# Optimization experiments

Hardware: AMD Instinct MI355X
Metric: run time of the kernel (lower is better)

The kernel has to match this reference:

```python
import jax, jax.numpy as jnp
import numpy as np

B, W, F = 64, 128, 64          # batch, window (node feat dim), n_features (nodes)
H, OUTW = 4, 128               # num_heads, out window size
NEG_SLOPE = 0.2                # LeakyReLU negative slope (alpha)


def setup_inputs() -> dict:
    key = jax.random.key(0)
    ks = jax.random.split(key, 6)
    scale_in = 1.0 / np.sqrt(W)
    scale_a = 1.0 / np.sqrt(OUTW)
    return {
        "x": jax.random.normal(ks[0], (B, W, F), dtype=jnp.float32),
        "W_src": jax.random.normal(ks[1], (H * OUTW, W), dtype=jnp.float32) * scale_in,
        "b_src": jnp.zeros((H * OUTW,), dtype=jnp.float32),
        "W_dst": jax.random.normal(ks[2], (H * OUTW, W), dtype=jnp.float32) * scale_in,
        "b_dst": jnp.zeros((H * OUTW,), dtype=jnp.float32),
        "attn": jax.random.normal(ks[3], (H, OUTW), dtype=jnp.float32) * scale_a,
    }


def reference(x, W_src, b_src, W_dst, b_dst, attn):
    # x: [B, W, F] -> node features nf: [B, F, W] (F nodes, W-dim features)
    nf = jnp.transpose(x, (0, 2, 1))
    b, f, w = nf.shape
    h, outw = attn.shape
    # GATv2 separate source/destination projections (share_weights=False)
    fs = (nf @ W_src.T + b_src).reshape(b, f, h, outw)  # [B, F, H, outW]
    fd = (nf @ W_dst.T + b_dst).reshape(b, f, h, outw)
    # additive score over complete graph with self-loops: e[b,i,j,h,d]
    s = fs[:, :, None, :, :] + fd[:, None, :, :, :]      # [B, src, dst, H, outW]
    e = jnp.where(s >= 0, s, NEG_SLOPE * s)              # LeakyReLU
    scores = jnp.einsum('bijhd,hd->bhij', e, attn)       # [B, H, src, dst]
    # edge softmax: normalize over incoming edges (sources) per destination
    a = jax.nn.softmax(scores, axis=2)
    # weighted scatter-sum aggregation at destinations
    out = jnp.einsum('bhij,bihd->bjhd', a, fs)           # [B, F, H, outW]
    out = out.mean(axis=2)                               # mean over heads -> [B, F, outW]
    return jnp.transpose(out, (0, 2, 1))                 # [B, outW, F]
```

## Files before the change

### kernel.cpp

```cpp
#include <hip/hip_runtime.h>
#include <math.h>

#define BB 64
#define WW 128
#define FF 64
#define HH 4
#define OW 128

__global__ __launch_bounds__(256) void gat_proj(
    const float* __restrict__ x,
    const float* __restrict__ Wsrc,
    const float* __restrict__ bsrc,
    const float* __restrict__ Wdst,
    const float* __restrict__ bdst,
    float* __restrict__ fs,
    float* __restrict__ fd)
{
    __shared__ float xl[64 * FF];
    __shared__ float wl[64 * 68];
    __shared__ float bl[64];

    const int b  = blockIdx.x >> 4;
    const int rt = blockIdx.x & 15;
    const bool is_src = rt < 8;
    const int rm0 = (rt & 7) * 64;

    const float* Wm = is_src ? Wsrc : Wdst;
    const float* bm = is_src ? bsrc : bdst;

    const int t  = threadIdx.x;
    const int f0 = (t & 15) * 4;
    const int r0 = (t >> 4) * 4;

    float acc[4][4] = {};

    for (int kp = 0; kp < 2; ++kp) {
        {
            const float4* xs = (const float4*)(x + (size_t)b * (WW * FF) + kp * 64 * FF);
            float4* xd = (float4*)xl;
            #pragma unroll
            for (int p = 0; p < 4; ++p)
                xd[p * 256 + t] = xs[p * 256 + t];
            float4* wd = (float4*)wl;
            #pragma unroll
            for (int p = 0; p < 4; ++p) {
                int idx = p * 256 + t;
                int r = idx >> 4, kq = idx & 15;
                wd[r * 17 + kq] =
                    *(const float4*)(Wm + (size_t)(rm0 + r) * WW + kp * 64 + kq * 4);
            }
            if (kp == 0 && t < 64) bl[t] = bm[rm0 + t];
        }
        __syncthreads();

        #pragma unroll
        for (int k0 = 0; k0 < 64; k0 += 4) {
            float4 xv[4], wv[4];
            #pragma unroll
            for (int kk = 0; kk < 4; ++kk)
                xv[kk] = *(const float4*)&xl[(k0 + kk) * FF + f0];
            #pragma unroll
            for (int rr = 0; rr < 4; ++rr)
                wv[rr] = *(const float4*)&wl[(r0 + rr) * 68 + k0];
            #pragma unroll
            for (int kk = 0; kk < 4; ++kk) {
                #pragma unroll
                for (int rr = 0; rr < 4; ++rr) {
                    const float wf = ((const float*)&wv[rr])[kk];
                    const float* xf = (const float*)&xv[kk];
                    acc[rr][0] = fmaf(xf[0], wf, acc[rr][0]);
                    acc[rr][1] = fmaf(xf[1], wf, acc[rr][1]);
                    acc[rr][2] = fmaf(xf[2], wf, acc[rr][2]);
                    acc[rr][3] = fmaf(xf[3], wf, acc[rr][3]);
                }
            }
        }
        __syncthreads();
    }

    const int h  = (rt & 7) >> 1;
    const int d0 = ((rt & 1) * 64) + r0;
    float* dst = (is_src ? fs : fd) + (((size_t)b * HH + h) * FF) * OW;
    float b0 = bl[r0 + 0], b1 = bl[r0 + 1], b2 = bl[r0 + 2], b3 = bl[r0 + 3];
    #pragma unroll
    for (int ff = 0; ff < 4; ++ff) {
        float4 o;
        o.x = acc[0][ff] + b0;
        o.y = acc[1][ff] + b1;
        o.z = acc[2][ff] + b2;
        o.w = acc[3][ff] + b3;
        *(float4*)&dst[(size_t)(f0 + ff) * OW + d0] = o;
    }
}

__global__ __launch_bounds__(256) void gat_attn(
    const float* __restrict__ fs,
    const float* __restrict__ fd,
    const float* __restrict__ attn,
    float* __restrict__ ws2)
{
    __shared__ float fsl[FF * 132];
    __shared__ float fdl[32 * 132];
    __shared__ float St[FF * 36];
    __shared__ float A6[OW], B4[OW];
    __shared__ float cs[FF], cd[32];
    __shared__ float redm[8][32];
    __shared__ float reds[8][32];
    __shared__ float invl[32];

    const int bx = blockIdx.x;
    const int jh = bx & 1;
    const int h  = (bx >> 1) & 3;
    const int b  = bx >> 3;
    const size_t bh = (size_t)b * HH + h;
    const int jbase = jh * 32;

    const int t    = threadIdx.x;
    const int wv   = t >> 6;
    const int lane = t & 63;

    {
        const float4* s = (const float4*)(fs + bh * (FF * OW));
        float4* d4 = (float4*)fsl;
        #pragma unroll
        for (int p = 0; p < 8; ++p) {
            int idx = p * 256 + t;
            int i = idx >> 5, kq = idx & 31;
            d4[i * 33 + kq] = s[idx];
        }
        const float4* fsrc = (const float4*)(fd + (bh * FF + jbase) * OW);
        float4* fdst = (float4*)fdl;
        #pragma unroll
        for (int p = 0; p < 4; ++p) {
            int idx = p * 256 + t;
            int j = idx >> 5, kq = idx & 31;
            fdst[j * 33 + kq] = fsrc[idx];
        }
        if (t < 128) {
            float a = attn[h * OW + t];
            A6[t] = 0.6f * a;
            B4[t] = 0.4f * a;
        }
    }
    __syncthreads();

    if (t < 64) {
        float s = 0.0f;
        #pragma unroll 8
        for (int c = 0; c < 32; ++c) {
            float4 fv = *(const float4*)&fsl[t * 132 + c * 4];
            float4 av = *(const float4*)&A6[c * 4];
            s = fmaf(fv.x, av.x, fmaf(fv.y, av.y, fmaf(fv.z, av.z, fmaf(fv.w, av.w, s))));
        }
        cs[t] = s;
    } else if (t < 96) {
        const int j = t - 64;
        float s = 0.0f;
        #pragma unroll 8
        for (int c = 0; c < 32; ++c) {
            float4 fv = *(const float4*)&fdl[j * 132 + c * 4];
            float4 av = *(const float4*)&A6[c * 4];
            s = fmaf(fv.x, av.x, fmaf(fv.y, av.y, fmaf(fv.z, av.z, fmaf(fv.w, av.w, s))));
        }
        cd[j] = s;
    }
    __syncthreads();

    const int jl0 = wv * 8;
    {
        float sc[8] = {};
        #pragma unroll 4
        for (int c = 0; c < 32; ++c) {
            const int d0 = c * 4;
            float4 fsv = *(const float4*)&fsl[lane * 132 + d0];
            float4 b4  = *(const float4*)&B4[d0];
            #pragma unroll
            for (int jj = 0; jj < 8; ++jj) {
                float4 fdv = *(const float4*)&fdl[(jl0 + jj) * 132 + d0];
                float r = sc[jj];
                r = fmaf(b4.x, fabsf(fsv.x + fdv.x), r);
                r = fmaf(b4.y, fabsf(fsv.y + fdv.y), r);
                r = fmaf(b4.z, fabsf(fsv.z + fdv.z), r);
                r = fmaf(b4.w, fabsf(fsv.w + fdv.w), r);
                sc[jj] = r;
            }
        }
        const float csl = cs[lane];
        float4 o0, o1;
        o0.x = sc[0] + csl + cd[jl0 + 0];
        o0.y = sc[1] + csl + cd[jl0 + 1];
        o0.z = sc[2] + csl + cd[jl0 + 2];
        o0.w = sc[3] + csl + cd[jl0 + 3];
        o1.x = sc[4] + csl + cd[jl0 + 4];
        o1.y = sc[5] + csl + cd[jl0 + 5];
        o1.z = sc[6] + csl + cd[jl0 + 6];
        o1.w = sc[7] + csl + cd[jl0 + 7];
        *(float4*)&St[lane * 36 + jl0]     = o0;
        *(float4*)&St[lane * 36 + jl0 + 4] = o1;
    }
    __syncthreads();

    {
        const int j = t & 31, st = t >> 5;
        const int i0 = st * 8;
        float m = St[i0 * 36 + j];
        #pragma unroll
        for (int k = 1; k < 8; ++k) m = fmaxf(m, St[(i0 + k) * 36 + j]);
        redm[st][j] = m;
    }
    __syncthreads();
    {
        const int j = t & 31, st = t >> 5;
        const int i0 = st * 8;
        float mj = redm[0][j];
        #pragma unroll
        for (int s2 = 1; s2 < 8; ++s2) mj = fmaxf(mj, redm[s2][j]);
        float ps = 0.0f;
        #pragma unroll
        for (int k = 0; k < 8; ++k) {
            float e = __expf(St[(i0 + k) * 36 + j] - mj);
            St[(i0 + k) * 36 + j] = e;
            ps += e;
        }
        reds[st][j] = ps;
    }
    __syncthreads();
    if (t < 32) {
        float l = 0.0f;
        #pragma unroll
        for (int s2 = 0; s2 < 8; ++s2) l += reds[s2][t];
        invl[t] = 0.25f / l;
    }
    __syncthreads();

    {
        const int dg = t & 7;
        const int jr = t >> 3;
        float ag[16] = {};
        for (int i = 0; i < FF; ++i) {
            const float p = St[i * 36 + jr];
            const float* fr = &fsl[i * 132 + dg * 4];
            float4 f0 = *(const float4*)(fr);
            float4 f1 = *(const float4*)(fr + 32);
            float4 f2 = *(const float4*)(fr + 64);
            float4 f3 = *(const float4*)(fr + 96);
            ag[0]  = fmaf(p, f0.x, ag[0]);  ag[1]  = fmaf(p, f0.y, ag[1]);
            ag[2]  = fmaf(p, f0.z, ag[2]);  ag[3]  = fmaf(p, f0.w, ag[3]);
            ag[4]  = fmaf(p, f1.x, ag[4]);  ag[5]  = fmaf(p, f1.y, ag[5]);
            ag[6]  = fmaf(p, f1.z, ag[6]);  ag[7]  = fmaf(p, f1.w, ag[7]);
            ag[8]  = fmaf(p, f2.x, ag[8]);  ag[9]  = fmaf(p, f2.y, ag[9]);
            ag[10] = fmaf(p, f2.z, ag[10]); ag[11] = fmaf(p, f2.w, ag[11]);
            ag[12] = fmaf(p, f3.x, ag[12]); ag[13] = fmaf(p, f3.y, ag[13]);
            ag[14] = fmaf(p, f3.z, ag[14]); ag[15] = fmaf(p, f3.w, ag[15]);
        }
        const float iv = invl[jr];
        float* wout = ws2 + (bh * FF + jbase + jr) * OW + dg * 4;
        #pragma unroll
        for (int q = 0; q < 4; ++q) {
            float4 o;
            o.x = ag[q * 4 + 0] * iv;
            o.y = ag[q * 4 + 1] * iv;
            o.z = ag[q * 4 + 2] * iv;
            o.w = ag[q * 4 + 3] * iv;
            *(float4*)&wout[q * 32] = o;
        }
    }
}

__global__ __launch_bounds__(256) void gat_reduce(
    const float* __restrict__ ws2,
    float* __restrict__ out)
{
    __shared__ float tl[16][132];
    const int b  = blockIdx.x >> 2;
    const int jg = blockIdx.x & 3;
    const int t  = threadIdx.x;

    const float* base = ws2 + ((size_t)b * HH * FF + jg * 16) * OW;
    #pragma unroll
    for (int p = 0; p < 2; ++p) {
        int idx = p * 256 + t;
        int j = idx >> 5, q = idx & 31;
        const float* src = base + (size_t)j * OW + q * 4;
        float4 s0 = *(const float4*)(src);
        float4 s1 = *(const float4*)(src + (size_t)FF * OW);
        float4 s2 = *(const float4*)(src + (size_t)2 * FF * OW);
        float4 s3 = *(const float4*)(src + (size_t)3 * FF * OW);
        float4 o;
        o.x = s0.x + s1.x + s2.x + s3.x;
        o.y = s0.y + s1.y + s2.y + s3.y;
        o.z = s0.z + s1.z + s2.z + s3.z;
        o.w = s0.w + s1.w + s2.w + s3.w;
        *(float4*)&tl[j][q * 4] = o;
    }
    __syncthreads();
    #pragma unroll
    for (int it = 0; it < 8; ++it) {
        int idx = it * 256 + t;
        int j = idx & 15, d = idx >> 4;
        out[((size_t)b * OW + d) * FF + jg * 16 + j] = tl[j][d];
    }
}

extern "C" void kernel_launch(void* const* d_in, const int* in_sizes, int n_in,
                              void* d_out, int out_size, void* d_ws, size_t ws_size,
                              hipStream_t stream) {
    const float* x    = (const float*)d_in[0];
    const float* Wsrc = (const float*)d_in[1];
    const float* bsrc = (const float*)d_in[2];
    const float* Wdst = (const float*)d_in[3];
    const float* bdst = (const float*)d_in[4];
    const float* attn = (const float*)d_in[5];
    float* out = (float*)d_out;

    const size_t SL = (size_t)BB * HH * FF * OW;
    float* fs  = (float*)d_ws;
    float* fd  = fs + SL;
    float* ws2 = fd + SL;

    gat_proj  <<<BB * 16,     256, 0, stream>>>(x, Wsrc, bsrc, Wdst, bdst, fs, fd);
    gat_attn  <<<BB * HH * 2, 256, 0, stream>>>(fs, fd, attn, ws2);
    gat_reduce<<<BB * 4,      256, 0, stream>>>(ws2, out);
}
```

Before: 114.9 us.

## Fuse projection, attention and head-reduction into one kernel with atomic output

Merges the three kernels into one kernel per (batch, head) block. Each block computes the src/dst projections straight into shared memory, which a union reuses for the attention stage, then handles all 64 destinations in a single 512-thread block. Head averaging becomes atomicAdd into a zeroed output. This drops the global round trips for fs/fd/ws2 and two kernel launches. In exchange it adds a memset, contention on the atomics, the output reduction order varies across heads, and there are fewer, larger blocks (256).

```diff
diff --git a/kernel.cpp b/kernel.cpp
--- a/kernel.cpp
+++ b/kernel.cpp
@@ -7,139 +7,108 @@
 #define HH 4
 #define OW 128
 
-__global__ __launch_bounds__(256) void gat_proj(
+
+struct GemmRegion {
+    float xq[32 * 64];
+    float wq[2 * 128 * 36];
+};
+struct AttnRegion {
+    float fsl[64 * 132];
+    float fdl[64 * 132];
+    float st[64 * 68];
+    float A6[OW], B4[OW];
+    float cs[FF], cd[FF];
+    float redm[8 * 64];
+    float reds[8 * 64];
+    float invl[64];
+};
+union SMem { GemmRegion g; AttnRegion a; };
+
+__global__ __launch_bounds__(512) void gat_fused(
     const float* __restrict__ x,
     const float* __restrict__ Wsrc,
     const float* __restrict__ bsrc,
     const float* __restrict__ Wdst,
     const float* __restrict__ bdst,
-    float* __restrict__ fs,
-    float* __restrict__ fd)
+    const float* __restrict__ attn,
+    float* __restrict__ out)
 {
-    __shared__ float xl[64 * FF];
-    __shared__ float wl[64 * 68];
-    __shared__ float bl[64];
-
-    const int b  = blockIdx.x >> 4;
-    const int rt = blockIdx.x & 15;
-    const bool is_src = rt < 8;
-    const int rm0 = (rt & 7) * 64;
-
-    const float* Wm = is_src ? Wsrc : Wdst;
-    const float* bm = is_src ? bsrc : bdst;
-
+    __shared__ __align__(16) SMem sm;
+    __shared__ float bl[2 * 128];
+
+    const int bx = blockIdx.x;
+    const int h  = bx & 3;
+    const int b  = bx >> 2;
     const int t  = threadIdx.x;
-    const int f0 = (t & 15) * 4;
-    const int r0 = (t >> 4) * 4;
-
-    float acc[4][4] = {};
-
-    for (int kp = 0; kp < 2; ++kp) {
+
+    const int m  = t >> 8;
+    const int i0 = (t & 15) * 4;
+    const int d0 = ((t >> 4) & 15) * 8;
+
+    if (t < 256) bl[t] = (t & 128 ? bdst : bsrc)[h * 128 + (t & 127)];
+
+    float acc[8][4] = {};
+
+    for (int kq = 0; kq < 4; ++kq) {
+        if (kq) __syncthreads();
         {
-            const float4* xs = (const float4*)(x + (size_t)b * (WW * FF) + kp * 64 * FF);
-            float4* xd = (float4*)xl;
-            #pragma unroll
-            for (int p = 0; p < 4; ++p)
-                xd[p * 256 + t] = xs[p * 256 + t];
-            float4* wd = (float4*)wl;
-            #pragma unroll
-            for (int p = 0; p < 4; ++p) {
-                int idx = p * 256 + t;
-                int r = idx >> 4, kq = idx & 15;
-                wd[r * 17 + kq] =
-                    *(const float4*)(Wm + (size_t)(rm0 + r) * WW + kp * 64 + kq * 4);
-            }
-            if (kp == 0 && t < 64) bl[t] = bm[rm0 + t];
+            const float4* xs = (const float4*)(x + ((size_t)b * WW + kq * 32) * FF);
+            ((float4*)sm.g.xq)[t] = xs[t];
+        }
+        #pragma unroll
+        for (int p = 0; p < 4; ++p) {
+            int idx = p * 512 + t;
+            int mm = idx >> 10, d = (idx >> 3) & 127, q = idx & 7;
+            const float* src = (mm ? Wdst : Wsrc)
+                             + (size_t)(h * 128 + d) * WW + kq * 32 + q * 4;
+            *(float4*)&sm.g.wq[(mm * 128 + d) * 36 + q * 4] = *(const float4*)src;
         }
         __syncthreads();
 
         #pragma unroll
-        for (int k0 = 0; k0 < 64; k0 += 4) {
-            float4 xv[4], wv[4];
+        for (int k0 = 0; k0 < 32; k0 += 4) {
+            float4 xv[4];
             #pragma unroll
             for (int kk = 0; kk < 4; ++kk)
-                xv[kk] = *(const float4*)&xl[(k0 + kk) * FF + f0];
-            #pragma unroll
-            for (int rr = 0; rr < 4; ++rr)
-                wv[rr] = *(const float4*)&wl[(r0 + rr) * 68 + k0];
+                xv[kk] = *(const float4*)&sm.g.xq[(k0 + kk) * 64 + i0];
+            float4 wv[8];
+            #pragma unroll
+            for (int dd = 0; dd < 8; ++dd)
+                wv[dd] = *(const float4*)&sm.g.wq[(m * 128 + d0 + dd) * 36 + k0];
             #pragma unroll
             for (int kk = 0; kk < 4; ++kk) {
+                const float* xf = (const float*)&xv[kk];
                 #pragma unroll
-                for (int rr = 0; rr < 4; ++rr) {
-                    const float wf = ((const float*)&wv[rr])[kk];
-                    const float* xf = (const float*)&xv[kk];
-                    acc[rr][0] = fmaf(xf[0], wf, acc[rr][0]);
-                    acc[rr][1] = fmaf(xf[1], wf, acc[rr][1]);
-                    acc[rr][2] = fmaf(xf[2], wf, acc[rr][2]);
-                    acc[rr][3] = fmaf(xf[3], wf, acc[rr][3]);
+                for (int dd = 0; dd < 8; ++dd) {
+                    const float wf = ((const float*)&wv[dd])[kk];
+                    acc[dd][0] = fmaf(xf[0], wf, acc[dd][0]);
+                    acc[dd][1] = fmaf(xf[1], wf, acc[dd][1]);
+                    acc[dd][2] = fmaf(xf[2], wf, acc[dd][2]);
+                    acc[dd][3] = fmaf(xf[3], wf, acc[dd][3]);
                 }
             }
         }
-        __syncthreads();
-    }
-
-    const int h  = (rt & 7) >> 1;
-    const int d0 = ((rt & 1) * 64) + r0;
-    float* dst = (is_src ? fs : fd) + (((size_t)b * HH + h) * FF) * OW;
-    float b0 = bl[r0 + 0], b1 = bl[r0 + 1], b2 = bl[r0 + 2], b3 = bl[r0 + 3];
-    #pragma unroll
-    for (int ff = 0; ff < 4; ++ff) {
-        float4 o;
-        o.x = acc[0][ff] + b0;
-        o.y = acc[1][ff] + b1;
-        o.z = acc[2][ff] + b2;
-        o.w = acc[3][ff] + b3;
-        *(float4*)&dst[(size_t)(f0 + ff) * OW + d0] = o;
-    }
-}
-
-__global__ __launch_bounds__(256) void gat_attn(
-    const float* __restrict__ fs,
-    const float* __restrict__ fd,
-    const float* __restrict__ attn,
-    float* __restrict__ ws2)
-{
-    __shared__ float fsl[FF * 132];
-    __shared__ float fdl[32 * 132];
-    __shared__ float St[FF * 36];
-    __shared__ float A6[OW], B4[OW];
-    __shared__ float cs[FF], cd[32];
-    __shared__ float redm[8][32];
-    __shared__ float reds[8][32];
-    __shared__ float invl[32];
-
-    const int bx = blockIdx.x;
-    const int jh = bx & 1;
-    const int h  = (bx >> 1) & 3;
-    const int b  = bx >> 3;
-    const size_t bh = (size_t)b * HH + h;
-    const int jbase = jh * 32;
-
-    const int t    = threadIdx.x;
-    const int wv   = t >> 6;
-    const int lane = t & 63;
-
-    {
-        const float4* s = (const float4*)(fs + bh * (FF * OW));
-        float4* d4 = (float4*)fsl;
-        #pragma unroll
-        for (int p = 0; p < 8; ++p) {
-            int idx = p * 256 + t;
-            int i = idx >> 5, kq = idx & 31;
-            d4[i * 33 + kq] = s[idx];
-        }
-        const float4* fsrc = (const float4*)(fd + (bh * FF + jbase) * OW);
-        float4* fdst = (float4*)fdl;
-        #pragma unroll
-        for (int p = 0; p < 4; ++p) {
-            int idx = p * 256 + t;
-            int j = idx >> 5, kq = idx & 31;
-            fdst[j * 33 + kq] = fsrc[idx];
+    }
+    __syncthreads();
+
+    {
+        float* dst = m ? sm.a.fdl : sm.a.fsl;
+        #pragma unroll
+        for (int ii = 0; ii < 4; ++ii) {
+            #pragma unroll
+            for (int dq = 0; dq < 2; ++dq) {
+                float4 o;
+                o.x = acc[dq * 4 + 0][ii] + bl[m * 128 + d0 + dq * 4 + 0];
+                o.y = acc[dq * 4 + 1][ii] + bl[m * 128 + d0 + dq * 4 + 1];
+                o.z = acc[dq * 4 + 2][ii] + bl[m * 128 + d0 + dq * 4 + 2];
+                o.w = acc[dq * 4 + 3][ii] + bl[m * 128 + d0 + dq * 4 + 3];
+                *(float4*)&dst[(i0 + ii) * 132 + d0 + dq * 4] = o;
+            }
         }
         if (t < 128) {
-            float a = attn[h * OW + t];
-            A6[t] = 0.6f * a;
-            B4[t] = 0.4f * a;
+            float av = attn[h * OW + t];
+            sm.a.A6[t] = 0.6f * av;
+            sm.a.B4[t] = 0.4f * av;
         }
     }
     __syncthreads();
@@ -148,35 +117,36 @@
         float s = 0.0f;
         #pragma unroll 8
         for (int c = 0; c < 32; ++c) {
-            float4 fv = *(const float4*)&fsl[t * 132 + c * 4];
-            float4 av = *(const float4*)&A6[c * 4];
+            float4 fv = *(const float4*)&sm.a.fsl[t * 132 + c * 4];
+            float4 av = *(const float4*)&sm.a.A6[c * 4];
             s = fmaf(fv.x, av.x, fmaf(fv.y, av.y, fmaf(fv.z, av.z, fmaf(fv.w, av.w, s))));
         }
-        cs[t] = s;
-    } else if (t < 96) {
+        sm.a.cs[t] = s;
+    } else if (t < 128) {
         const int j = t - 64;
         float s = 0.0f;
         #pragma unroll 8
         for (int c = 0; c < 32; ++c) {
-            float4 fv = *(const float4*)&fdl[j * 132 + c * 4];
-            float4 av = *(const float4*)&A6[c * 4];
+            float4 fv = *(const float4*)&sm.a.fdl[j * 132 + c * 4];
+            float4 av = *(const float4*)&sm.a.A6[c * 4];
             s = fmaf(fv.x, av.x, fmaf(fv.y, av.y, fmaf(fv.z, av.z, fmaf(fv.w, av.w, s))));
         }
-        cd[j] = s;
-    }
-    __syncthreads();
-
-    const int jl0 = wv * 8;
-    {
+        sm.a.cd[j] = s;
+    }
+    __syncthreads();
+
+    {
+        const int lane = t & 63;
+        const int jl0  = (t >> 6) * 8;
         float sc[8] = {};
         #pragma unroll 4
         for (int c = 0; c < 32; ++c) {
-            const int d0 = c * 4;
-            float4 fsv = *(const float4*)&fsl[lane * 132 + d0];
-            float4 b4  = *(const float4*)&B4[d0];
+            const int dd0 = c * 4;
+            float4 fsv = *(const float4*)&sm.a.fsl[lane * 132 + dd0];
+            float4 b4  = *(const float4*)&sm.a.B4[dd0];
             #pragma unroll
             for (int jj = 0; jj < 8; ++jj) {
-                float4 fdv = *(const float4*)&fdl[(jl0 + jj) * 132 + d0];
+                float4 fdv = *(const float4*)&sm.a.fdl[(jl0 + jj) * 132 + dd0];
                 float r = sc[jj];
                 r = fmaf(b4.x, fabsf(fsv.x + fdv.x), r);
                 r = fmaf(b4.y, fabsf(fsv.y + fdv.y), r);
@@ -185,65 +155,65 @@
                 sc[jj] = r;
             }
         }
-        const float csl = cs[lane];
+        const float csl = sm.a.cs[lane];
         float4 o0, o1;
-        o0.x = sc[0] + csl + cd[jl0 + 0];
-        o0.y = sc[1] + csl + cd[jl0 + 1];
-        o0.z = sc[2] + csl + cd[jl0 + 2];
-        o0.w = sc[3] + csl + cd[jl0 + 3];
-        o1.x = sc[4] + csl + cd[jl0 + 4];
-        o1.y = sc[5] + csl + cd[jl0 + 5];
-        o1.z = sc[6] + csl + cd[jl0 + 6];
-        o1.w = sc[7] + csl + cd[jl0 + 7];
-        *(float4*)&St[lane * 36 + jl0]     = o0;
-        *(float4*)&St[lane * 36 + jl0 + 4] = o1;
-    }
-    __syncthreads();
-
-    {
-        const int j = t & 31, st = t >> 5;
-        const int i0 = st * 8;
-        float m = St[i0 * 36 + j];
-        #pragma unroll
-        for (int k = 1; k < 8; ++k) m = fmaxf(m, St[(i0 + k) * 36 + j]);
-        redm[st][j] = m;
-    }
-    __syncthreads();
-    {
-        const int j = t & 31, st = t >> 5;
-        const int i0 = st * 8;
-        float mj = redm[0][j];
-        #pragma unroll
-        for (int s2 = 1; s2 < 8; ++s2) mj = fmaxf(mj, redm[s2][j]);
+        o0.x = sc[0] + csl + sm.a.cd[jl0 + 0];
+        o0.y = sc[1] + csl + sm.a.cd[jl0 + 1];
+        o0.z = sc[2] + csl + sm.a.cd[jl0 + 2];
+        o0.w = sc[3] + csl + sm.a.cd[jl0 + 3];
+        o1.x = sc[4] + csl + sm.a.cd[jl0 + 4];
+        o1.y = sc[5] + csl + sm.a.cd[jl0 + 5];
+        o1.z = sc[6] + csl + sm.a.cd[jl0 + 6];
+        o1.w = sc[7] + csl + sm.a.cd[jl0 + 7];
+        *(float4*)&sm.a.st[lane * 68 + jl0]     = o0;
+        *(float4*)&sm.a.st[lane * 68 + jl0 + 4] = o1;
+    }
+    __syncthreads();
+
+    {
+        const int j = t & 63, st8 = t >> 6;
+        const int i0s = st8 * 8;
+        float mx = sm.a.st[i0s * 68 + j];
+        #pragma unroll
+        for (int k = 1; k < 8; ++k) mx = fmaxf(mx, sm.a.st[(i0s + k) * 68 + j]);
+        sm.a.redm[st8 * 64 + j] = mx;
+    }
+    __syncthreads();
+    {
+        const int j = t & 63, st8 = t >> 6;
+        const int i0s = st8 * 8;
+        float mj = sm.a.redm[j];
+        #pragma unroll
+        for (int s2 = 1; s2 < 8; ++s2) mj = fmaxf(mj, sm.a.redm[s2 * 64 + j]);
         float ps = 0.0f;
         #pragma unroll
         for (int k = 0; k < 8; ++k) {
-            float e = __expf(St[(i0 + k) * 36 + j] - mj);
-            St[(i0 + k) * 36 + j] = e;
+            float e = __expf(sm.a.st[(i0s + k) * 68 + j] - mj);
+            sm.a.st[(i0s + k) * 68 + j] = e;
             ps += e;
         }
-        reds[st][j] = ps;
-    }
-    __syncthreads();
-    if (t < 32) {
+        sm.a.reds[st8 * 64 + j] = ps;
+    }
+    __syncthreads();
+    if (t < 64) {
         float l = 0.0f;
         #pragma unroll
-        for (int s2 = 0; s2 < 8; ++s2) l += reds[s2][t];
-        invl[t] = 0.25f / l;
-    }
-    __syncthreads();
-
-    {
-        const int dg = t & 7;
-        const int jr = t >> 3;
+        for (int s2 = 0; s2 < 8; ++s2) l += sm.a.reds[s2 * 64 + t];
+        sm.a.invl[t] = 0.25f / l;
+    }
+    __syncthreads();
+
+    {
+        const int j = t & 63, dblk = t >> 6;
         float ag[16] = {};
+        #pragma unroll 4
         for (int i = 0; i < FF; ++i) {
-            const float p = St[i * 36 + jr];
-            const float* fr = &fsl[i * 132 + dg * 4];
+            const float p = sm.a.st[i * 68 + j];
+            const float* fr = &sm.a.fsl[i * 132 + dblk * 16];
             float4 f0 = *(const float4*)(fr);
-            float4 f1 = *(const float4*)(fr + 32);
-            float4 f2 = *(const float4*)(fr + 64);
-            float4 f3 = *(const float4*)(fr + 96);
+            float4 f1 = *(const float4*)(fr + 4);
+            float4 f2 = *(const float4*)(fr + 8);
+            float4 f3 = *(const float4*)(fr + 12);
             ag[0]  = fmaf(p, f0.x, ag[0]);  ag[1]  = fmaf(p, f0.y, ag[1]);
             ag[2]  = fmaf(p, f0.z, ag[2]);  ag[3]  = fmaf(p, f0.w, ag[3]);
             ag[4]  = fmaf(p, f1.x, ag[4]);  ag[5]  = fmaf(p, f1.y, ag[5]);
@@ -253,52 +223,11 @@
             ag[12] = fmaf(p, f3.x, ag[12]); ag[13] = fmaf(p, f3.y, ag[13]);
             ag[14] = fmaf(p, f3.z, ag[14]); ag[15] = fmaf(p, f3.w, ag[15]);
         }
-        const float iv = invl[jr];
-        float* wout = ws2 + (bh * FF + jbase + jr) * OW + dg * 4;
-        #pragma unroll
-        for (int q = 0; q < 4; ++q) {
-            float4 o;
-            o.x = ag[q * 4 + 0] * iv;
-            o.y = ag[q * 4 + 1] * iv;
-            o.z = ag[q * 4 + 2] * iv;
-            o.w = ag[q * 4 + 3] * iv;
-            *(float4*)&wout[q * 32] = o;
-        }
-    }
-}
-
-__global__ __launch_bounds__(256) void gat_reduce(
-    const float* __restrict__ ws2,
-    float* __restrict__ out)
-{
-    __shared__ float tl[16][132];
-    const int b  = blockIdx.x >> 2;
-    const int jg = blockIdx.x & 3;
-    const int t  = threadIdx.x;
-
-    const float* base = ws2 + ((size_t)b * HH * FF + jg * 16) * OW;
-    #pragma unroll
-    for (int p = 0; p < 2; ++p) {
-        int idx = p * 256 + t;
-        int j = idx >> 5, q = idx & 31;
-        const float* src = base + (size_t)j * OW + q * 4;
-        float4 s0 = *(const float4*)(src);
-        float4 s1 = *(const float4*)(src + (size_t)FF * OW);
-        float4 s2 = *(const float4*)(src + (size_t)2 * FF * OW);
-        float4 s3 = *(const float4*)(src + (size_t)3 * FF * OW);
-        float4 o;
-        o.x = s0.x + s1.x + s2.x + s3.x;
-        o.y = s0.y + s1.y + s2.y + s3.y;
-        o.z = s0.z + s1.z + s2.z + s3.z;
-        o.w = s0.w + s1.w + s2.w + s3.w;
-        *(float4*)&tl[j][q * 4] = o;
-    }
-    __syncthreads();
-    #pragma unroll
-    for (int it = 0; it < 8; ++it) {
-        int idx = it * 256 + t;
-        int j = idx & 15, d = idx >> 4;
-        out[((size_t)b * OW + d) * FF + jg * 16 + j] = tl[j][d];
+        const float iv = sm.a.invl[j];
+        float* ob = out + ((size_t)b * OW + dblk * 16) * FF + j;
+        #pragma unroll
+        for (int e = 0; e < 16; ++e)
+            atomicAdd(ob + e * FF, ag[e] * iv);
     }
 }
 
@@ -311,14 +240,8 @@
     const float* Wdst = (const float*)d_in[3];
     const float* bdst = (const float*)d_in[4];
     const float* attn = (const float*)d_in[5];
-    float* out = (float*)d_out;
-
-    const size_t SL = (size_t)BB * HH * FF * OW;
-    float* fs  = (float*)d_ws;
-    float* fd  = fs + SL;
-    float* ws2 = fd + SL;
-
-    gat_proj  <<<BB * 16,     256, 0, stream>>>(x, Wsrc, bsrc, Wdst, bdst, fs, fd);
-    gat_attn  <<<BB * HH * 2, 256, 0, stream>>>(fs, fd, attn, ws2);
-    gat_reduce<<<BB * 4,      256, 0, stream>>>(ws2, out);
+
+    hipMemsetAsync(d_out, 0, (size_t)out_size, stream);
+    gat_fused<<<BB * HH, 512, 0, stream>>>(x, Wsrc, bsrc, Wdst, bdst, attn,
+                                           (float*)d_out);
 }
```

Result: faster. 106.6 us (-7.3%).
